# Kernel tuning notes

Hardware: AMD Instinct MI355X
Metric: run time of the kernel (lower is better)

Reference implementation:

```python
import jax, jax.numpy as jnp
import numpy as np

N, V, H, LAT, OUT = 256, 256, 256, 64, 128
EPS = 1e-5

def setup_inputs() -> dict:
    key = jax.random.key(0)
    ks = jax.random.split(key, 16)
    s = lambda fan_in: 1.0 / np.sqrt(fan_in)
    gin = 2 * H + LAT  # GAT input size
    return {
        "obs": jax.random.normal(ks[0], (N, V, 5), jnp.float32),
        "high_intention": jax.random.normal(ks[1], (N, V, LAT), jnp.float32),
        "Ws": jax.random.uniform(ks[2], (2, H), jnp.float32, -s(2), s(2)),
        "bs": jax.random.uniform(ks[3], (H,), jnp.float32, -s(2), s(2)),
        "Wv": jax.random.uniform(ks[4], (2, H), jnp.float32, -s(2), s(2)),
        "bv": jax.random.uniform(ks[5], (H,), jnp.float32, -s(2), s(2)),
        "Wg": jax.random.uniform(ks[6], (gin, H), jnp.float32, -s(gin), s(gin)),
        "a_w": jax.random.uniform(ks[7], (2 * H,), jnp.float32, -s(2 * H), s(2 * H)),
        "W1": jax.random.uniform(ks[8], (2 * H, H), jnp.float32, -s(2 * H), s(2 * H)),
        "b1": jax.random.uniform(ks[9], (H,), jnp.float32, -s(2 * H), s(2 * H)),
        "g1": jnp.ones((H,), jnp.float32),
        "be1": jnp.zeros((H,), jnp.float32),
        "W2": jax.random.uniform(ks[10], (H, OUT), jnp.float32, -s(H), s(H)),
        "b2": jax.random.uniform(ks[11], (OUT,), jnp.float32, -s(H), s(H)),
        "g2": jnp.ones((OUT,), jnp.float32),
        "be2": jnp.zeros((OUT,), jnp.float32),
    }

def _batchnorm(x, g, b):
    # training-mode BatchNorm1d: batch stats, biased variance
    m = x.mean(0)
    v = x.var(0)
    return g * (x - m) / jnp.sqrt(v + EPS) + b

def reference(obs, high_intention, Ws, bs, Wv, bv, Wg, a_w, W1, b1, g1, be1, W2, b2, g2, be2):
    se = jax.nn.relu(obs[:, :, 1:3] @ Ws + bs)   # [N,V,H]
    ve = jax.nn.relu(obs[:, :, 3:5] @ Wv + bv)   # [N,V,H]
    comb = jnp.concatenate([se, ve, high_intention], axis=-1)  # [N,V,2H+LAT]
    h = comb @ Wg                                 # [N,V,H]
    hdim = Ws.shape[1]
    a1, a2 = a_w[:hdim], a_w[hdim:]
    # e_ij = leaky_relu(a . [h_i, h_j]) = leaky_relu(h_i.a1 + h_j.a2)
    e = jax.nn.leaky_relu((h @ a1)[:, :, None] + (h @ a2)[:, None, :], 0.01)  # [N,V,V]
    att = jax.nn.softmax(e, axis=2)
    h_prime = jnp.einsum('nij,njh->nih', att, h)  # [N,V,H]
    cf = jnp.concatenate([h_prime, se], axis=-1).reshape(-1, 2 * hdim)
    x = jax.nn.relu(_batchnorm(cf @ W1 + b1, g1, be1))
    x = jax.nn.relu(_batchnorm(x @ W2 + b2, g2, be2))
    return x.reshape(obs.shape[0], obs.shape[1], -1)
```

## Files before the change

### kernel.cpp

```cpp
#include <hip/hip_runtime.h>
#include <math.h>

namespace {

constexpr int kH = 256, kOut = 128;
constexpr int kNV = 65536;
constexpr float kEps = 1e-5f;

typedef __attribute__((ext_vector_type(8))) short bf16x8;
typedef __attribute__((ext_vector_type(4))) float f32x4;
typedef unsigned int u32;

__device__ inline short f2bf(float f) {
  union { float f; u32 u; } v; v.f = f;
  u32 r = v.u + 0x7fffu + ((v.u >> 16) & 1u);
  return (short)(r >> 16);
}
__device__ inline float bf2f(short s) {
  union { float f; u32 u; } v; v.u = ((u32)(unsigned short)s) << 16; return v.f;
}

__global__ __launch_bounds__(256) void kpack(
    const float* __restrict__ Wg, const float* __restrict__ W1,
    const float* __restrict__ W2, const float* __restrict__ a_w,
    short* __restrict__ wgp, short* __restrict__ w1p, short* __restrict__ w2p,
    short* __restrict__ wgab, float* __restrict__ st)
{
  const int bid = blockIdx.x, t = threadIdx.x;
  if (bid >= 152) {
    const int b = bid - 152;
    if (t < 144) {
      const int col = t & 1, k = b * 72 + (t >> 1);
      if (k < 576) {
        const float* rowp = Wg + (size_t)k * 256;
        const float* ap = a_w + col * 256;
        float s0 = 0.f, s1 = 0.f, s2 = 0.f, s3 = 0.f;
        for (int c = 0; c < 256; c += 4) {
          s0 = fmaf(rowp[c+0], ap[c+0], s0);
          s1 = fmaf(rowp[c+1], ap[c+1], s1);
          s2 = fmaf(rowp[c+2], ap[c+2], s2);
          s3 = fmaf(rowp[c+3], ap[c+3], s3);
        }
        const int ks = k >> 5, r = k & 31, hq = r >> 3, e = r & 7;
        wgab[((ks*2 + col)*4 + hq)*8 + e] = f2bf((s0 + s1) + (s2 + s3));
      }
    }
    return;
  }
  if (bid == 0) {
#pragma unroll
    for (int i = 0; i < 6; ++i) st[i*256 + t] = 0.f;
  }
  const int uid = bid * 256 + t;
  const float* src; short* dst; int N; int u;
  if (uid < 18432)            { src = Wg; dst = wgp; N = 256; u = uid; }
  else if (uid < 34816)       { src = W1; dst = w1p; N = 256; u = uid - 18432; }
  else if (uid < 38912)       { src = W2; dst = w2p; N = 128; u = uid - 34816; }
  else return;
  const int lane = u & 63, ctkt = u >> 6;
  const int nct = N >> 4;
  const int kt = ctkt / nct, ct = ctkt % nct;
  const int row = kt * 32 + (lane >> 4) * 8;
  const int col = ct * 16 + (lane & 15);
  bf16x8 ov;
#pragma unroll
  for (int e = 0; e < 8; ++e) ov[e] = f2bf(src[(size_t)(row + e) * N + col]);
  *reinterpret_cast<bf16x8*>(dst + (size_t)u * 8) = ov;
}

__global__ __launch_bounds__(256, 4) void k1_encode(
    const float* __restrict__ obs, const float* __restrict__ hin,
    const float* __restrict__ Ws, const float* __restrict__ bs,
    const float* __restrict__ Wv, const float* __restrict__ bv,
    const short* __restrict__ wgp, const short* __restrict__ wgab,
    short* __restrict__ hpack, float* __restrict__ ha1, float* __restrict__ ha2)
{
  __shared__ __align__(16) short comb[32][584];
  __shared__ float obs_s[32][4];
  const int t = threadIdx.x;
  const int xcd = blockIdx.x & 7, ib = blockIdx.x >> 3;
  const int workid = xcd * 256 + ib;
  const int r0 = workid * 32;
  const int w = t >> 6, lane = t & 63, lo = lane & 15, hq = lane >> 4;

  const short* wB = wgp + ((size_t)(w*4)*64 + lane)*8;
  bf16x8 bb[4];
#pragma unroll
  for (int ct = 0; ct < 4; ++ct)
    bb[ct] = *reinterpret_cast<const bf16x8*>(wB + ct*512);

  if (t < 128) obs_s[t >> 2][t & 3] = obs[(size_t)(r0 + (t >> 2)) * 5 + 1 + (t & 3)];
#pragma unroll
  for (int jj = 0; jj < 2; ++jj) {
    const int f = jj * 1024 + t * 4;
    const int row = f >> 6, c = f & 63;
    const float4 v = *reinterpret_cast<const float4*>(hin + (size_t)r0 * 64 + f);
    short4 o;
    o.x = f2bf(v.x); o.y = f2bf(v.y); o.z = f2bf(v.z); o.w = f2bf(v.w);
    *reinterpret_cast<short4*>(&comb[row][512 + c]) = o;
  }
  const float ws0 = Ws[t], ws1 = Ws[256 + t], bsv = bs[t];
  const float wv0 = Wv[t], wv1 = Wv[256 + t], bvv = bv[t];
  __syncthreads();
  for (int r = 0; r < 32; ++r) {
    const float o1 = obs_s[r][0], o2 = obs_s[r][1], o3 = obs_s[r][2], o4 = obs_s[r][3];
    const float sv = fmaf(o2, ws1, fmaf(o1, ws0, bsv));
    comb[r][t] = f2bf(fmaxf(sv, 0.f));
    const float vv = fmaf(o4, wv1, fmaf(o3, wv0, bvv));
    comb[r][256 + t] = f2bf(fmaxf(vv, 0.f));
  }
  __syncthreads();

  f32x4 acc[2][4];
  f32x4 accE[2];
#pragma unroll
  for (int rt = 0; rt < 2; ++rt) {
    accE[rt] = (f32x4){0.f, 0.f, 0.f, 0.f};
#pragma unroll
    for (int ct = 0; ct < 4; ++ct) acc[rt][ct] = (f32x4){0.f, 0.f, 0.f, 0.f};
  }

#pragma unroll
  for (int ks = 0; ks < 18; ++ks) {
    bf16x8 bn[4];
    if (ks < 17) {
#pragma unroll
      for (int ct = 0; ct < 4; ++ct)
        bn[ct] = *reinterpret_cast<const bf16x8*>(wB + (ks+1)*8192 + ct*512);
    }
    bf16x8 a[2];
#pragma unroll
    for (int rt = 0; rt < 2; ++rt)
      a[rt] = *reinterpret_cast<const bf16x8*>(&comb[rt*16 + lo][ks*32 + hq*8]);
#pragma unroll
    for (int rt = 0; rt < 2; ++rt)
#pragma unroll
      for (int ct = 0; ct < 4; ++ct)
        acc[rt][ct] = __builtin_amdgcn_mfma_f32_16x16x32_bf16(a[rt], bb[ct], acc[rt][ct], 0, 0, 0);
    if (w == 0) {
      bf16x8 be;
      if (lo < 2)
        be = *reinterpret_cast<const bf16x8*>(wgab + ((ks*2 + lo)*4 + hq)*8);
      else
        be = (bf16x8){0,0,0,0,0,0,0,0};
#pragma unroll
      for (int rt = 0; rt < 2; ++rt)
        accE[rt] = __builtin_amdgcn_mfma_f32_16x16x32_bf16(a[rt], be, accE[rt], 0, 0, 0);
    }
    if (ks < 17) {
#pragma unroll
      for (int ct = 0; ct < 4; ++ct) bb[ct] = bn[ct];
    }
  }
  if (w == 0 && lo < 2) {
    float* dst = (lo == 0) ? ha1 : ha2;
#pragma unroll
    for (int rt = 0; rt < 2; ++rt)
#pragma unroll
      for (int q = 0; q < 4; ++q)
        dst[r0 + rt*16 + hq*4 + q] = accE[rt][q];
  }
  __syncthreads();

  short* pimg = reinterpret_cast<short*>(&comb[0][0]);
#pragma unroll
  for (int rt = 0; rt < 2; ++rt)
#pragma unroll
    for (int ct = 0; ct < 4; ++ct) {
      const int base = (((w*4 + ct)*64) + (rt*2 + (hq>>1))*16 + lo)*8 + (hq&1)*4;
      short4 val;
      val.x = f2bf(acc[rt][ct][0]); val.y = f2bf(acc[rt][ct][1]);
      val.z = f2bf(acc[rt][ct][2]); val.w = f2bf(acc[rt][ct][3]);
      *reinterpret_cast<short4*>(pimg + base) = val;
    }
  __syncthreads();

  short* dst = hpack + (size_t)workid * 8192;
#pragma unroll
  for (int j = 0; j < 4; ++j)
    *reinterpret_cast<bf16x8*>(dst + j*2048 + t*8) =
        *reinterpret_cast<const bf16x8*>(pimg + j*2048 + t*8);
}

__global__ __launch_bounds__(256, 4) void k23_attn_fc1(
    const float* __restrict__ ha1g, const float* __restrict__ ha2g,
    const short* __restrict__ hpack, const float* __restrict__ obs,
    const float* __restrict__ Ws, const float* __restrict__ bs,
    const short* __restrict__ w1p, short* __restrict__ y, float* __restrict__ st)
{
  __shared__ __align__(16) short attimg[64][264];
  __shared__ float ws_s[768];
  __shared__ float ha2_s[256];
  __shared__ float ha1_s[64], rd_s[64];
  __shared__ float red[4][64];
  __shared__ float obs_s[64][2];
  const int t = threadIdx.x;
  const int xcd = blockIdx.x & 7, ib = blockIdx.x >> 3;
  const int workid = xcd * 128 + ib;
  const int r0 = workid * 64;
  const int n = r0 >> 8;
  const int w = t >> 6, lane = t & 63, lo = lane & 15, hq = lane >> 4;

  const short* bB = hpack + (size_t)n*65536 + ((size_t)(w*4)*64 + lane)*8;
  const short* w1B = w1p + ((size_t)(w*4)*64 + lane)*8;
  bf16x8 bb[4];
#pragma unroll
  for (int ct = 0; ct < 4; ++ct)
    bb[ct] = *reinterpret_cast<const bf16x8*>(bB + ct*512);

  ws_s[t] = Ws[t]; ws_s[256 + t] = Ws[256 + t]; ws_s[512 + t] = bs[t];
  ha2_s[t] = ha2g[n*256 + t];
  if (t < 64) ha1_s[t] = ha1g[r0 + t];
  if (t < 128) obs_s[t >> 1][t & 1] = obs[(size_t)(r0 + (t >> 1)) * 5 + 1 + (t & 1)];
  __syncthreads();

  const int rr = t & 63, seg = t >> 6;
  {
    const float a1 = ha1_s[rr];
    float sum = 0.f;
    for (int c8 = 0; c8 < 8; ++c8) {
      bf16x8 pk;
#pragma unroll
      for (int e = 0; e < 8; ++e) {
        float x = a1 + ha2_s[seg*64 + c8*8 + e];
        x = fmaxf(x, 0.01f * x);
        const float ev = __expf(x);
        sum += ev;
        pk[e] = f2bf(ev);
      }
      *reinterpret_cast<bf16x8*>(&attimg[rr][seg*64 + c8*8]) = pk;
    }
    red[seg][rr] = sum;
  }
  __syncthreads();
  if (t < 64) rd_s[t] = 1.f / (red[0][t] + red[1][t] + red[2][t] + red[3][t]);
  __syncthreads();

  f32x4 acc[4][4];
#pragma unroll
  for (int rt = 0; rt < 4; ++rt)
#pragma unroll
    for (int ct = 0; ct < 4; ++ct) acc[rt][ct] = (f32x4){0.f, 0.f, 0.f, 0.f};

  {
    for (int ks = 0; ks < 8; ++ks) {
      bf16x8 bn[4];
      if (ks < 7) {
#pragma unroll
        for (int ct = 0; ct < 4; ++ct)
          bn[ct] = *reinterpret_cast<const bf16x8*>(bB + (ks+1)*8192 + ct*512);
      }
      bf16x8 a[4];
#pragma unroll
      for (int rt = 0; rt < 4; ++rt)
        a[rt] = *reinterpret_cast<const bf16x8*>(&attimg[rt*16 + lo][ks*32 + hq*8]);
#pragma unroll
      for (int rt = 0; rt < 4; ++rt)
#pragma unroll
        for (int ct = 0; ct < 4; ++ct)
          acc[rt][ct] = __builtin_amdgcn_mfma_f32_16x16x32_bf16(a[rt], bb[ct], acc[rt][ct], 0, 0, 0);
      if (ks < 7) {
#pragma unroll
        for (int ct = 0; ct < 4; ++ct) bb[ct] = bn[ct];
      }
    }
  }
  bf16x8 bbw[4];
#pragma unroll
  for (int ct = 0; ct < 4; ++ct)
    bbw[ct] = *reinterpret_cast<const bf16x8*>(w1B + ct*512);
  __syncthreads();

#pragma unroll
  for (int rt = 0; rt < 4; ++rt)
#pragma unroll
    for (int q = 0; q < 4; ++q) {
      const int row = rt*16 + hq*4 + q;
      const float sc = rd_s[row];
#pragma unroll
      for (int ct = 0; ct < 4; ++ct)
        attimg[row][w*64 + ct*16 + lo] = f2bf(acc[rt][ct][q] * sc);
    }
  __syncthreads();

  f32x4 accY[4][4];
#pragma unroll
  for (int rt = 0; rt < 4; ++rt)
#pragma unroll
    for (int ct = 0; ct < 4; ++ct) accY[rt][ct] = (f32x4){0.f, 0.f, 0.f, 0.f};
  {
    for (int ks = 0; ks < 8; ++ks) {
      bf16x8 bn[4];
      if (ks < 7) {
#pragma unroll
        for (int ct = 0; ct < 4; ++ct)
          bn[ct] = *reinterpret_cast<const bf16x8*>(w1B + (ks+1)*8192 + ct*512);
      }
      bf16x8 a[4];
#pragma unroll
      for (int rt = 0; rt < 4; ++rt)
        a[rt] = *reinterpret_cast<const bf16x8*>(&attimg[rt*16 + lo][ks*32 + hq*8]);
#pragma unroll
      for (int rt = 0; rt < 4; ++rt)
#pragma unroll
        for (int ct = 0; ct < 4; ++ct)
          accY[rt][ct] = __builtin_amdgcn_mfma_f32_16x16x32_bf16(a[rt], bbw[ct], accY[rt][ct], 0, 0, 0);
      if (ks < 7) {
#pragma unroll
        for (int ct = 0; ct < 4; ++ct) bbw[ct] = bn[ct];
      }
    }
  }
  bf16x8 bbv[4];
#pragma unroll
  for (int ct = 0; ct < 4; ++ct)
    bbv[ct] = *reinterpret_cast<const bf16x8*>(w1B + 8*8192 + ct*512);
  __syncthreads();

  {
    const float o1 = obs_s[rr][0], o2 = obs_s[rr][1];
    for (int c8 = 0; c8 < 8; ++c8) {
      const int c = seg*64 + c8*8;
      bf16x8 pk;
#pragma unroll
      for (int e = 0; e < 8; ++e) {
        const float sv = fmaf(o2, ws_s[256 + c + e], fmaf(o1, ws_s[c + e], ws_s[512 + c + e]));
        pk[e] = f2bf(fmaxf(sv, 0.f));
      }
      *reinterpret_cast<bf16x8*>(&attimg[rr][c]) = pk;
    }
  }
  __syncthreads();

  {
    for (int ks = 0; ks < 8; ++ks) {
      bf16x8 bn[4];
      if (ks < 7) {
#pragma unroll
        for (int ct = 0; ct < 4; ++ct)
          bn[ct] = *reinterpret_cast<const bf16x8*>(w1B + (ks+9)*8192 + ct*512);
      }
      bf16x8 a[4];
#pragma unroll
      for (int rt = 0; rt < 4; ++rt)
        a[rt] = *reinterpret_cast<const bf16x8*>(&attimg[rt*16 + lo][ks*32 + hq*8]);
#pragma unroll
      for (int rt = 0; rt < 4; ++rt)
#pragma unroll
        for (int ct = 0; ct < 4; ++ct)
          accY[rt][ct] = __builtin_amdgcn_mfma_f32_16x16x32_bf16(a[rt], bbv[ct], accY[rt][ct], 0, 0, 0);
      if (ks < 7) {
#pragma unroll
        for (int ct = 0; ct < 4; ++ct) bbv[ct] = bn[ct];
      }
    }
  }

  float sm[4] = {0,0,0,0}, ssm[4] = {0,0,0,0};
#pragma unroll
  for (int rt = 0; rt < 4; ++rt)
#pragma unroll
    for (int q = 0; q < 4; ++q)
#pragma unroll
      for (int ct = 0; ct < 4; ++ct) {
        const float v = accY[rt][ct][q];
        sm[ct] += v; ssm[ct] += v * v;
      }
#pragma unroll
  for (int off = 16; off < 64; off <<= 1)
#pragma unroll
    for (int ct = 0; ct < 4; ++ct) {
      sm[ct] += __shfl_xor(sm[ct], off);
      ssm[ct] += __shfl_xor(ssm[ct], off);
    }
  if (hq == 0)
#pragma unroll
    for (int ct = 0; ct < 4; ++ct) {
      const int col = w*64 + ct*16 + lo;
      atomicAdd(&st[col], sm[ct]);
      atomicAdd(&st[256 + col], ssm[ct]);
    }
  __syncthreads();

#pragma unroll
  for (int rt = 0; rt < 4; ++rt)
#pragma unroll
    for (int q = 0; q < 4; ++q) {
      const int row = rt*16 + hq*4 + q;
#pragma unroll
      for (int ct = 0; ct < 4; ++ct)
        attimg[row][w*64 + ct*16 + lo] = f2bf(accY[rt][ct][q]);
    }
  __syncthreads();
  const short* img = &attimg[0][0];
#pragma unroll
  for (int j = 0; j < 8; ++j) {
    const int f = j*2048 + t*8, row = f >> 8, col = f & 255;
    *reinterpret_cast<bf16x8*>(y + (size_t)(r0 + row)*256 + col) =
        *reinterpret_cast<const bf16x8*>(img + row*264 + col);
  }
}

__global__ __launch_bounds__(256) void k5_z(
    const short* __restrict__ y, const short* __restrict__ w2p,
    const float* __restrict__ g1, const float* __restrict__ be1,
    float* __restrict__ st, short* __restrict__ zb)
{
  __shared__ __align__(16) short xs[64][264];
  __shared__ float sc_s[256], sh_s[256];
  const int t = threadIdx.x;
  const int xcd = blockIdx.x & 7, ib = blockIdx.x >> 3;
  const int workid = xcd * 128 + ib;
  const int r0 = workid * 64;
  const int w = t >> 6, lane = t & 63, lo = lane & 15, hq = lane >> 4;

  const short* w2B = w2p + ((size_t)(w*2)*64 + lane)*8;
  bf16x8 bb[2];
#pragma unroll
  for (int ct = 0; ct < 2; ++ct)
    bb[ct] = *reinterpret_cast<const bf16x8*>(w2B + ct*512);

  {
    const float mean = st[t] * (1.f / kNV);
    const float var  = st[256 + t] * (1.f / kNV) - mean * mean;
    const float sc   = g1[t] / sqrtf(var + kEps);
    sc_s[t] = sc; sh_s[t] = be1[t] - mean * sc;
  }
  __syncthreads();
#pragma unroll
  for (int j = 0; j < 8; ++j) {
    const int f = j*2048 + t*8, row = f >> 8, col = f & 255;
    bf16x8 v = *reinterpret_cast<const bf16x8*>(y + (size_t)(r0 + row)*256 + col);
    bf16x8 ov;
#pragma unroll
    for (int e = 0; e < 8; ++e) {
      const float fv = fmaf(bf2f(v[e]), sc_s[col + e], sh_s[col + e]);
      ov[e] = f2bf(fmaxf(fv, 0.f));
    }
    *reinterpret_cast<bf16x8*>(&xs[row][col]) = ov;
  }
  __syncthreads();

  f32x4 acc[4][2];
#pragma unroll
  for (int rt = 0; rt < 4; ++rt)
#pragma unroll
    for (int ct = 0; ct < 2; ++ct) acc[rt][ct] = (f32x4){0.f, 0.f, 0.f, 0.f};

  {
    for (int ks = 0; ks < 8; ++ks) {
      bf16x8 bn[2];
      if (ks < 7) {
#pragma unroll
        for (int ct = 0; ct < 2; ++ct)
          bn[ct] = *reinterpret_cast<const bf16x8*>(w2B + (ks+1)*4096 + ct*512);
      }
      bf16x8 a[4];
#pragma unroll
      for (int rt = 0; rt < 4; ++rt)
        a[rt] = *reinterpret_cast<const bf16x8*>(&xs[rt*16 + lo][ks*32 + hq*8]);
#pragma unroll
      for (int rt = 0; rt < 4; ++rt)
#pragma unroll
        for (int ct = 0; ct < 2; ++ct)
          acc[rt][ct] = __builtin_amdgcn_mfma_f32_16x16x32_bf16(a[rt], bb[ct], acc[rt][ct], 0, 0, 0);
      if (ks < 7) {
#pragma unroll
        for (int ct = 0; ct < 2; ++ct) bb[ct] = bn[ct];
      }
    }
  }

  float sm[2] = {0,0}, ssm[2] = {0,0};
#pragma unroll
  for (int rt = 0; rt < 4; ++rt)
#pragma unroll
    for (int q = 0; q < 4; ++q)
#pragma unroll
      for (int ct = 0; ct < 2; ++ct) {
        const float v = acc[rt][ct][q];
        sm[ct] += v; ssm[ct] += v * v;
      }
#pragma unroll
  for (int off = 16; off < 64; off <<= 1)
#pragma unroll
    for (int ct = 0; ct < 2; ++ct) {
      sm[ct] += __shfl_xor(sm[ct], off);
      ssm[ct] += __shfl_xor(ssm[ct], off);
    }
  if (hq == 0)
#pragma unroll
    for (int ct = 0; ct < 2; ++ct) {
      const int col = w*32 + ct*16 + lo;
      atomicAdd(&st[1024 + col], sm[ct]);
      atomicAdd(&st[1152 + col], ssm[ct]);
    }
  __syncthreads();

  short* zimg = reinterpret_cast<short*>(&xs[0][0]);
#pragma unroll
  for (int rt = 0; rt < 4; ++rt)
#pragma unroll
    for (int q = 0; q < 4; ++q) {
      const int row = rt*16 + hq*4 + q;
#pragma unroll
      for (int ct = 0; ct < 2; ++ct)
        zimg[row*136 + w*32 + ct*16 + lo] = f2bf(acc[rt][ct][q]);
    }
  __syncthreads();
#pragma unroll
  for (int j = 0; j < 4; ++j) {
    const int f = j*2048 + t*8, row = f >> 7, col = f & 127;
    *reinterpret_cast<bf16x8*>(zb + (size_t)(r0 + row)*128 + col) =
        *reinterpret_cast<const bf16x8*>(zimg + row*136 + col);
  }
}

__global__ __launch_bounds__(256) void k7_out(
    const short* __restrict__ zb, const float* __restrict__ st,
    const float* __restrict__ g2, const float* __restrict__ be2,
    float* __restrict__ out)
{
  __shared__ float sc_s[128], sh_s[128];
  const int t = threadIdx.x;
  const int xcd = blockIdx.x & 7, ib = blockIdx.x >> 3;
  const int workid = xcd * 256 + ib;
  if (t < 128) {
    const float mean = st[1024 + t] * (1.f / kNV);
    const float var  = st[1152 + t] * (1.f / kNV) - mean * mean;
    const float sc   = g2[t] / sqrtf(var + kEps);
    sc_s[t] = sc; sh_s[t] = be2[t] - mean * sc;
  }
  __syncthreads();
#pragma unroll
  for (int j = 0; j < 2; ++j) {
    const size_t u = (size_t)workid * 512 + j*256 + t;
    bf16x8 v = *reinterpret_cast<const bf16x8*>(zb + u*8);
    const int col = ((int)u & 15) * 8;
    float4 r0, r1;
    r0.x = fmaxf(fmaf(bf2f(v[0]), sc_s[col+0], sh_s[col+0]), 0.f);
    r0.y = fmaxf(fmaf(bf2f(v[1]), sc_s[col+1], sh_s[col+1]), 0.f);
    r0.z = fmaxf(fmaf(bf2f(v[2]), sc_s[col+2], sh_s[col+2]), 0.f);
    r0.w = fmaxf(fmaf(bf2f(v[3]), sc_s[col+3], sh_s[col+3]), 0.f);
    r1.x = fmaxf(fmaf(bf2f(v[4]), sc_s[col+4], sh_s[col+4]), 0.f);
    r1.y = fmaxf(fmaf(bf2f(v[5]), sc_s[col+5], sh_s[col+5]), 0.f);
    r1.z = fmaxf(fmaf(bf2f(v[6]), sc_s[col+6], sh_s[col+6]), 0.f);
    r1.w = fmaxf(fmaf(bf2f(v[7]), sc_s[col+7], sh_s[col+7]), 0.f);
    *reinterpret_cast<float4*>(out + u*8)     = r0;
    *reinterpret_cast<float4*>(out + u*8 + 4) = r1;
  }
}

}

extern "C" void kernel_launch(void* const* d_in, const int* in_sizes, int n_in,
                              void* d_out, int out_size, void* d_ws, size_t ws_size,
                              hipStream_t stream) {
  const float* obs = (const float*)d_in[0];
  const float* hin = (const float*)d_in[1];
  const float* Ws  = (const float*)d_in[2];
  const float* bs  = (const float*)d_in[3];
  const float* Wv  = (const float*)d_in[4];
  const float* bv  = (const float*)d_in[5];
  const float* Wg  = (const float*)d_in[6];
  const float* a_w = (const float*)d_in[7];
  const float* W1  = (const float*)d_in[8];
  const float* g1  = (const float*)d_in[10];
  const float* be1 = (const float*)d_in[11];
  const float* W2  = (const float*)d_in[12];
  const float* g2  = (const float*)d_in[14];
  const float* be2 = (const float*)d_in[15];

  char* base = (char*)d_ws;
  short* hpack = (short*)(base);
  short* y     = (short*)(base + 33554432);
  short* zb    = (short*)(base + 67108864);
  float* ha1   = (float*)(base + 83886080);
  float* ha2   = (float*)(base + 84148224);
  float* st    = (float*)(base + 84410368);
  short* wgp   = (short*)(base + 84416512);
  short* w1p   = (short*)(base + 84711424);
  short* w2p   = (short*)(base + 84973568);
  short* wgab  = (short*)(base + 85039104);
  float* out   = (float*)d_out;

  kpack       <<<160,  256, 0, stream>>>(Wg, W1, W2, a_w, wgp, w1p, w2p, wgab, st);
  k1_encode   <<<2048, 256, 0, stream>>>(obs, hin, Ws, bs, Wv, bv, wgp, wgab, hpack, ha1, ha2);
  k23_attn_fc1<<<1024, 256, 0, stream>>>(ha1, ha2, hpack, obs, Ws, bs, w1p, y, st);
  k5_z        <<<1024, 256, 0, stream>>>(y, w2p, g1, be1, st, zb);
  k7_out      <<<2048, 256, 0, stream>>>(zb, st, g2, be2, out);
}
```

Measured before the change: 138.7 us.

## Move se@W1 second-half GEMM into encode kernel and pass via bf16 buffer

The se half of the FC1 GEMM (se @ W1[256:512]) is now computed in k1_encode, where se is already in shared memory. It is written to a new bf16 buffer in MFMA accumulator layout, and k23 preloads it as the initial accumulator. This removes the recompute of se, a shared-memory rewrite, two syncs and a GEMM phase from the attention kernel. In exchange it adds global traffic for the partial result and an extra bf16 rounding of the partial sum.

```diff
diff --git a/kernel.cpp b/kernel.cpp
--- a/kernel.cpp
+++ b/kernel.cpp
@@ -73,7 +73,9 @@
     const float* __restrict__ Ws, const float* __restrict__ bs,
     const float* __restrict__ Wv, const float* __restrict__ bv,
     const short* __restrict__ wgp, const short* __restrict__ wgab,
-    short* __restrict__ hpack, float* __restrict__ ha1, float* __restrict__ ha2)
+    const short* __restrict__ w1p,
+    short* __restrict__ hpack, float* __restrict__ ha1, float* __restrict__ ha2,
+    short* __restrict__ y2p)
 {
   __shared__ __align__(16) short comb[32][584];
   __shared__ float obs_s[32][4];
@@ -83,12 +85,6 @@
   const int r0 = workid * 32;
   const int w = t >> 6, lane = t & 63, lo = lane & 15, hq = lane >> 4;
 
-  const short* wB = wgp + ((size_t)(w*4)*64 + lane)*8;
-  bf16x8 bb[4];
-#pragma unroll
-  for (int ct = 0; ct < 4; ++ct)
-    bb[ct] = *reinterpret_cast<const bf16x8*>(wB + ct*512);
-
   if (t < 128) obs_s[t >> 2][t & 3] = obs[(size_t)(r0 + (t >> 2)) * 5 + 1 + (t & 3)];
 #pragma unroll
   for (int jj = 0; jj < 2; ++jj) {
@@ -119,6 +115,12 @@
 #pragma unroll
     for (int ct = 0; ct < 4; ++ct) acc[rt][ct] = (f32x4){0.f, 0.f, 0.f, 0.f};
   }
+
+  const short* wB = wgp + ((size_t)(w*4)*64 + lane)*8;
+  bf16x8 bb[4];
+#pragma unroll
+  for (int ct = 0; ct < 4; ++ct)
+    bb[ct] = *reinterpret_cast<const bf16x8*>(wB + ct*512);
 
 #pragma unroll
   for (int ks = 0; ks < 18; ++ks) {
@@ -160,6 +162,40 @@
       for (int q = 0; q < 4; ++q)
         dst[r0 + rt*16 + hq*4 + q] = accE[rt][q];
   }
+
+  {
+    f32x4 accY2[2][4];
+#pragma unroll
+    for (int rt = 0; rt < 2; ++rt)
+#pragma unroll
+      for (int ct = 0; ct < 4; ++ct) accY2[rt][ct] = (f32x4){0.f, 0.f, 0.f, 0.f};
+    const short* w1B = w1p + ((size_t)(w*4)*64 + lane)*8;
+    for (int ks = 0; ks < 8; ++ks) {
+      bf16x8 by[4];
+#pragma unroll
+      for (int ct = 0; ct < 4; ++ct)
+        by[ct] = *reinterpret_cast<const bf16x8*>(w1B + (ks+8)*8192 + ct*512);
+      bf16x8 a[2];
+#pragma unroll
+      for (int rt = 0; rt < 2; ++rt)
+        a[rt] = *reinterpret_cast<const bf16x8*>(&comb[rt*16 + lo][ks*32 + hq*8]);
+#pragma unroll
+      for (int rt = 0; rt < 2; ++rt)
+#pragma unroll
+        for (int ct = 0; ct < 4; ++ct)
+          accY2[rt][ct] = __builtin_amdgcn_mfma_f32_16x16x32_bf16(a[rt], by[ct], accY2[rt][ct], 0, 0, 0);
+    }
+#pragma unroll
+    for (int rt = 0; rt < 2; ++rt)
+#pragma unroll
+      for (int ct = 0; ct < 4; ++ct) {
+        short4 v;
+        v.x = f2bf(accY2[rt][ct][0]); v.y = f2bf(accY2[rt][ct][1]);
+        v.z = f2bf(accY2[rt][ct][2]); v.w = f2bf(accY2[rt][ct][3]);
+        *reinterpret_cast<short4*>(
+            y2p + (size_t)workid*8192 + (((w*4 + ct)*2 + rt)*64 + lane)*4) = v;
+      }
+  }
   __syncthreads();
 
   short* pimg = reinterpret_cast<short*>(&comb[0][0]);
@@ -184,16 +220,13 @@
 
 __global__ __launch_bounds__(256, 4) void k23_attn_fc1(
     const float* __restrict__ ha1g, const float* __restrict__ ha2g,
-    const short* __restrict__ hpack, const float* __restrict__ obs,
-    const float* __restrict__ Ws, const float* __restrict__ bs,
-    const short* __restrict__ w1p, short* __restrict__ y, float* __restrict__ st)
+    const short* __restrict__ hpack, const short* __restrict__ w1p,
+    const short* __restrict__ y2p, short* __restrict__ y, float* __restrict__ st)
 {
   __shared__ __align__(16) short attimg[64][264];
-  __shared__ float ws_s[768];
   __shared__ float ha2_s[256];
   __shared__ float ha1_s[64], rd_s[64];
   __shared__ float red[4][64];
-  __shared__ float obs_s[64][2];
   const int t = threadIdx.x;
   const int xcd = blockIdx.x & 7, ib = blockIdx.x >> 3;
   const int workid = xcd * 128 + ib;
@@ -208,10 +241,8 @@
   for (int ct = 0; ct < 4; ++ct)
     bb[ct] = *reinterpret_cast<const bf16x8*>(bB + ct*512);
 
-  ws_s[t] = Ws[t]; ws_s[256 + t] = Ws[256 + t]; ws_s[512 + t] = bs[t];
   ha2_s[t] = ha2g[n*256 + t];
   if (t < 64) ha1_s[t] = ha1g[r0 + t];
-  if (t < 128) obs_s[t >> 1][t & 1] = obs[(size_t)(r0 + (t >> 1)) * 5 + 1 + (t & 1)];
   __syncthreads();
 
   const int rr = t & 63, seg = t >> 6;
@@ -265,6 +296,15 @@
       }
     }
   }
+  short4 yp[4][4];
+#pragma unroll
+  for (int rt4 = 0; rt4 < 4; ++rt4)
+#pragma unroll
+    for (int ct = 0; ct < 4; ++ct) {
+      const int tile = rt4 >> 1, rtk = rt4 & 1;
+      yp[rt4][ct] = *reinterpret_cast<const short4*>(
+          y2p + (size_t)(workid*2 + tile)*8192 + (((w*4 + ct)*2 + rtk)*64 + lane)*4);
+    }
   bf16x8 bbw[4];
 #pragma unroll
   for (int ct = 0; ct < 4; ++ct)
@@ -285,9 +325,12 @@
 
   f32x4 accY[4][4];
 #pragma unroll
-  for (int rt = 0; rt < 4; ++rt)
-#pragma unroll
-    for (int ct = 0; ct < 4; ++ct) accY[rt][ct] = (f32x4){0.f, 0.f, 0.f, 0.f};
+  for (int rt4 = 0; rt4 < 4; ++rt4)
+#pragma unroll
+    for (int ct = 0; ct < 4; ++ct) {
+      const short4 v = yp[rt4][ct];
+      accY[rt4][ct] = (f32x4){bf2f(v.x), bf2f(v.y), bf2f(v.z), bf2f(v.w)};
+    }
   {
     for (int ks = 0; ks < 8; ++ks) {
       bf16x8 bn[4];
@@ -308,50 +351,6 @@
       if (ks < 7) {
 #pragma unroll
         for (int ct = 0; ct < 4; ++ct) bbw[ct] = bn[ct];
-      }
-    }
-  }
-  bf16x8 bbv[4];
-#pragma unroll
-  for (int ct = 0; ct < 4; ++ct)
-    bbv[ct] = *reinterpret_cast<const bf16x8*>(w1B + 8*8192 + ct*512);
-  __syncthreads();
-
-  {
-    const float o1 = obs_s[rr][0], o2 = obs_s[rr][1];
-    for (int c8 = 0; c8 < 8; ++c8) {
-      const int c = seg*64 + c8*8;
-      bf16x8 pk;
-#pragma unroll
-      for (int e = 0; e < 8; ++e) {
-        const float sv = fmaf(o2, ws_s[256 + c + e], fmaf(o1, ws_s[c + e], ws_s[512 + c + e]));
-        pk[e] = f2bf(fmaxf(sv, 0.f));
-      }
-      *reinterpret_cast<bf16x8*>(&attimg[rr][c]) = pk;
-    }
-  }
-  __syncthreads();
-
-  {
-    for (int ks = 0; ks < 8; ++ks) {
-      bf16x8 bn[4];
-      if (ks < 7) {
-#pragma unroll
-        for (int ct = 0; ct < 4; ++ct)
-          bn[ct] = *reinterpret_cast<const bf16x8*>(w1B + (ks+9)*8192 + ct*512);
-      }
-      bf16x8 a[4];
-#pragma unroll
-      for (int rt = 0; rt < 4; ++rt)
-        a[rt] = *reinterpret_cast<const bf16x8*>(&attimg[rt*16 + lo][ks*32 + hq*8]);
-#pragma unroll
-      for (int rt = 0; rt < 4; ++rt)
-#pragma unroll
-        for (int ct = 0; ct < 4; ++ct)
-          accY[rt][ct] = __builtin_amdgcn_mfma_f32_16x16x32_bf16(a[rt], bbv[ct], accY[rt][ct], 0, 0, 0);
-      if (ks < 7) {
-#pragma unroll
-        for (int ct = 0; ct < 4; ++ct) bbv[ct] = bn[ct];
       }
     }
   }
@@ -582,11 +581,13 @@
   short* w1p   = (short*)(base + 84711424);
   short* w2p   = (short*)(base + 84973568);
   short* wgab  = (short*)(base + 85039104);
+  short* y2p   = (short*)(base + 85041664);
   float* out   = (float*)d_out;
 
   kpack       <<<160,  256, 0, stream>>>(Wg, W1, W2, a_w, wgp, w1p, w2p, wgab, st);
-  k1_encode   <<<2048, 256, 0, stream>>>(obs, hin, Ws, bs, Wv, bv, wgp, wgab, hpack, ha1, ha2);
-  k23_attn_fc1<<<1024, 256, 0, stream>>>(ha1, ha2, hpack, obs, Ws, bs, w1p, y, st);
+  k1_encode   <<<2048, 256, 0, stream>>>(obs, hin, Ws, bs, Wv, bv, wgp, wgab, w1p,
+                                         hpack, ha1, ha2, y2p);
+  k23_attn_fc1<<<1024, 256, 0, stream>>>(ha1, ha2, hpack, w1p, y2p, y, st);
   k5_z        <<<1024, 256, 0, stream>>>(y, w2p, g1, be1, st, zb);
   k7_out      <<<2048, 256, 0, stream>>>(zb, st, g2, be2, out);
 }
```

New measurement: 155.0 us. +11.7%, slower.
